# Optimization experiments

Hardware: AMD Instinct MI355X
Metric: run time of the kernel (lower is better)

Reference implementation:

```python
import jax, jax.numpy as jnp
import numpy as np

P, B, FEAT, HID, ATTN, NHEAD = 4096, 32, 512, 512, 512, 8
HD = ATTN // NHEAD  # 64


def setup_inputs() -> dict:
    key = jax.random.key(0)
    ks = jax.random.split(key, 12)
    s = lambda n: 1.0 / np.sqrt(n)
    return {
        "last_hidden": jax.random.normal(ks[0], (1, B, HID), jnp.float32),
        "encoder_outputs": jax.random.normal(ks[1], (P, B, FEAT), jnp.float32),
        # outer projections (stored [in, out]; torch Linear is x @ W.T + b)
        "Wa_w": jax.random.uniform(ks[2], (FEAT, ATTN), jnp.float32, -s(FEAT), s(FEAT)),
        "Wa_b": jax.random.uniform(ks[3], (ATTN,), jnp.float32, -s(FEAT), s(FEAT)),
        "Ua_w": jax.random.uniform(ks[4], (HID, ATTN), jnp.float32, -s(HID), s(HID)),
        "Ua_b": jax.random.uniform(ks[5], (ATTN,), jnp.float32, -s(HID), s(HID)),
        # inner Attention(head_attn_size, head_attn_size, head_attn_size)
        "Wa2_w": jax.random.uniform(ks[6], (HD, HD), jnp.float32, -s(HD), s(HD)),
        "Wa2_b": jax.random.uniform(ks[7], (HD,), jnp.float32, -s(HD), s(HD)),
        "Ua2_w": jax.random.uniform(ks[8], (HD, HD), jnp.float32, -s(HD), s(HD)),
        "Ua2_b": jax.random.uniform(ks[9], (HD,), jnp.float32, -s(HD), s(HD)),
        "va_w": jax.random.uniform(ks[10], (HD, 1), jnp.float32, -s(HD), s(HD)),
        "va_b": jax.random.uniform(ks[11], (1,), jnp.float32, -s(HD), s(HD)),
        "nhead": NHEAD,
    }


def reference(last_hidden, encoder_outputs, Wa_w, Wa_b, Ua_w, Ua_b,
              Wa2_w, Wa2_b, Ua2_w, Ua2_b, va_w, va_b, nhead):
    p, b = encoder_outputs.shape[:2]
    enc = encoder_outputs @ Wa_w + Wa_b            # [P,B,A]
    hid = last_hidden @ Ua_w + Ua_b                # [1,B,A]
    hd = enc.shape[-1] // nhead
    enc = enc.reshape(p, b, nhead, hd)             # [P,B,nh,hd]
    hid = hid.reshape(1, b, nhead, hd)             # [1,B,nh,hd]
    # inner Bahdanau attention
    a = jnp.tanh((enc @ Wa2_w + Wa2_b) + (hid @ Ua2_w + Ua2_b))
    scores = a @ va_w + va_b                       # [P,B,nh,1]
    weights = jax.nn.softmax(scores, axis=0)       # softmax over pixels
    context = jnp.sum(weights * enc, axis=0, keepdims=True)  # [1,B,nh,hd]
    weight = jnp.mean(weights, axis=-2)            # mean over heads -> [P,B,1]
    context = context.reshape(1, b, nhead * hd)    # [1,B,A]
    return context, weight
```

## Files before the change

### kernel.cpp

```cpp
#include <hip/hip_runtime.h>
#include <hip/hip_bf16.h>

#define PDIM 4096
#define BDIM 32
#define MDIM (PDIM*BDIM)
#define KDIM 512
#define NDIM 512
#define NH   8
#define HD   64

typedef __attribute__((ext_vector_type(4))) float f32x4;
typedef __attribute__((ext_vector_type(8))) short bf16x8;

__device__ __forceinline__ unsigned short f2bf(float f) {
  unsigned u = __float_as_uint(f);
  u += 0x7fffu + ((u >> 16) & 1u);
  return (unsigned short)(u >> 16);
}
__device__ __forceinline__ float bf2f(unsigned short u) {
  return __uint_as_float(((unsigned)u) << 16);
}

__device__ __forceinline__ float fast_tanh(float x) {
  x = fminf(fmaxf(x, -15.f), 15.f);
  float e = __expf(2.f * x);
  return __fdividef(e - 1.f, e + 1.f);
}

#define GLOAD_LDS16(g, l) __builtin_amdgcn_global_load_lds( \
    (const __attribute__((address_space(1))) void*)(g),     \
    (__attribute__((address_space(3))) void*)(l), 16, 0, 0)

__global__ __launch_bounds__(256) void cvt_k(
    const float* __restrict__ x, unsigned short* __restrict__ xbf) {
  size_t i = ((size_t)blockIdx.x * 256 + threadIdx.x) * 8;
  float4 a = *(const float4*)(x + i);
  float4 b = *(const float4*)(x + i + 4);
  ushort4 o0; o0.x = f2bf(a.x); o0.y = f2bf(a.y); o0.z = f2bf(a.z); o0.w = f2bf(a.w);
  ushort4 o1; o1.x = f2bf(b.x); o1.y = f2bf(b.y); o1.z = f2bf(b.z); o1.w = f2bf(b.w);
  *(ushort4*)(xbf + i) = o0;
  *(ushort4*)(xbf + i + 4) = o1;
}

__global__ __launch_bounds__(512) void hub_k(
    const float* __restrict__ lh, const float* __restrict__ Ua,
    const float* __restrict__ Ua_b, const float* __restrict__ Ua2,
    const float* __restrict__ Ua2_b, const float* __restrict__ Wa_b,
    const float* __restrict__ Wa2, const float* __restrict__ Wa2_b,
    float* __restrict__ ubf) {
  int b = blockIdx.x, tid = threadIdx.x;
  __shared__ float ls[512];
  __shared__ float hs[512];
  ls[tid] = lh[b*512 + tid];
  __syncthreads();
  float s = Ua_b[tid];
  #pragma unroll 8
  for (int k = 0; k < 512; ++k)
    s += ls[k] * Ua[(size_t)k*512 + tid];
  hs[tid] = s;
  __syncthreads();
  int h = tid >> 6, j = tid & 63;
  float u = Ua2_b[j] + Wa2_b[j];
  #pragma unroll 4
  for (int k = 0; k < 64; ++k) {
    u += hs[h*64 + k] * Ua2[k*64 + j];
    u += Wa_b[h*64 + k] * Wa2[k*64 + j];
  }
  ubf[b*512 + tid] = u;
}

__global__ __launch_bounds__(256) void wft_k(
    const float* __restrict__ Wa, const float* __restrict__ Wa2,
    unsigned short* __restrict__ WfT) {
  int n = blockIdx.x, tid = threadIdx.x;
  int h = n >> 6, j = n & 63;
  __shared__ float w2[64];
  if (tid < 64) w2[tid] = Wa2[tid*64 + j];
  __syncthreads();
  for (int k = tid; k < 512; k += 256) {
    float s = 0.f;
    #pragma unroll 8
    for (int kk = 0; kk < 64; ++kk)
      s += Wa[(size_t)k*512 + h*64 + kk] * w2[kk];
    WfT[(size_t)n*512 + k] = f2bf(s);
  }
}

__global__ __launch_bounds__(256, 4) void gemm_score_k(
    const unsigned short* __restrict__ xbf, const unsigned short* __restrict__ WfT,
    const float* __restrict__ ubf, const float* __restrict__ va_w,
    const float* __restrict__ va_b, float* __restrict__ scores) {
  __shared__ __align__(16) unsigned short sm[16384];
  unsigned short* As = sm;
  unsigned short* Bs = sm + 8192;
  int tid = threadIdx.x;
  int orig = blockIdx.x;
  int wg = (orig & 7) * 512 + (orig >> 3);
  int bn = wg & 3, bm = wg >> 2;
  int m0 = bm*128, n0 = bn*128;
  int lane = tid & 63, w = tid >> 6;
  int quad = lane >> 4, l16 = lane & 15;
  int wr = w >> 1, wc = w & 1;
  int xr = (l16 & 7) << 4;
  f32x4 acc[4][4] = {};

  for (int k0 = 0; k0 < KDIM; k0 += 64) {
    __syncthreads();
    #pragma unroll
    for (int i = 0; i < 4; ++i) {
      int c = i*256 + tid;
      int r = c >> 3, kc = (c & 7) ^ (r & 7);
      GLOAD_LDS16(xbf + (size_t)(m0 + r)*512 + k0 + kc*8, As + (size_t)c*8);
    }
    #pragma unroll
    for (int i = 0; i < 4; ++i) {
      int c = i*256 + tid;
      int r = c >> 3, kc = (c & 7) ^ (r & 7);
      GLOAD_LDS16(WfT + (size_t)(n0 + r)*512 + k0 + kc*8, Bs + (size_t)c*8);
    }
    __syncthreads();
    #pragma unroll
    for (int kk = 0; kk < 64; kk += 32) {
      int kc = (kk >> 3) + quad;
      bf16x8 af[4], bfr[4];
      #pragma unroll
      for (int ti = 0; ti < 4; ++ti) {
        int row = 64*wr + 16*ti + l16;
        af[ti] = *(const bf16x8*)((const char*)As + ((row*128 + kc*16) ^ xr));
      }
      #pragma unroll
      for (int tj = 0; tj < 4; ++tj) {
        int row = 64*wc + 16*tj + l16;
        bfr[tj] = *(const bf16x8*)((const char*)Bs + ((row*128 + kc*16) ^ xr));
      }
      #pragma unroll
      for (int ti = 0; ti < 4; ++ti)
        #pragma unroll
        for (int tj = 0; tj < 4; ++tj)
          acc[ti][tj] = __builtin_amdgcn_mfma_f32_16x16x32_bf16(
              af[ti], bfr[tj], acc[ti][tj], 0, 0, 0);
    }
  }

  __syncthreads();
  float* ubf_s = (float*)sm;
  #pragma unroll
  for (int t = 0; t < 16; ++t) {
    int idx = t*256 + tid;
    int b = idx >> 7, c = idx & 127;
    ubf_s[b*129 + c] = ubf[b*512 + n0 + c];
  }
  __syncthreads();

  int head = bn*2 + wc;
  float va_r[4];
  #pragma unroll
  for (int tj = 0; tj < 4; ++tj) va_r[tj] = va_w[16*tj + l16];
  float vb = va_b[0];
  #pragma unroll
  for (int ti = 0; ti < 4; ++ti) {
    #pragma unroll
    for (int r = 0; r < 4; ++r) {
      int row_loc = 64*wr + 16*ti + 4*quad + r;
      int b31 = row_loc & 31;
      float s = 0.f;
      #pragma unroll
      for (int tj = 0; tj < 4; ++tj) {
        float xa = acc[ti][tj][r] + ubf_s[b31*129 + 64*wc + 16*tj + l16];
        s += fast_tanh(xa) * va_r[tj];
      }
      s += __shfl_xor(s, 1); s += __shfl_xor(s, 2);
      s += __shfl_xor(s, 4); s += __shfl_xor(s, 8);
      if (l16 == 0) {
        int m = m0 + row_loc;
        scores[((size_t)head*32 + (m & 31))*4096 + (m >> 5)] = s + vb;
      }
    }
  }
}

__global__ __launch_bounds__(256) void softmax_k(
    const float* __restrict__ sc, float* __restrict__ w) {
  int bh = blockIdx.x;
  int tid = threadIdx.x;
  const float* row = sc + (size_t)bh*4096;
  float4 v[4];
  float mx = -1e30f;
  #pragma unroll
  for (int i = 0; i < 4; ++i) {
    v[i] = *(const float4*)(row + (size_t)(i*256 + tid)*4);
    mx = fmaxf(mx, fmaxf(fmaxf(v[i].x, v[i].y), fmaxf(v[i].z, v[i].w)));
  }
  #pragma unroll
  for (int m = 1; m < 64; m <<= 1) mx = fmaxf(mx, __shfl_xor(mx, m));
  __shared__ float redm[4], reds[4];
  int wid = tid >> 6, lane = tid & 63;
  if (lane == 0) redm[wid] = mx;
  __syncthreads();
  mx = fmaxf(fmaxf(redm[0], redm[1]), fmaxf(redm[2], redm[3]));
  float sum = 0.f;
  #pragma unroll
  for (int i = 0; i < 4; ++i) {
    v[i].x = __expf(v[i].x - mx); v[i].y = __expf(v[i].y - mx);
    v[i].z = __expf(v[i].z - mx); v[i].w = __expf(v[i].w - mx);
    sum += v[i].x + v[i].y + v[i].z + v[i].w;
  }
  #pragma unroll
  for (int m = 1; m < 64; m <<= 1) sum += __shfl_xor(sum, m);
  if (lane == 0) reds[wid] = sum;
  __syncthreads();
  sum = reds[0] + reds[1] + reds[2] + reds[3];
  float inv = 1.f / sum;
  float* dst = w + (size_t)bh*4096;
  #pragma unroll
  for (int i = 0; i < 4; ++i) {
    float4 o; o.x = v[i].x*inv; o.y = v[i].y*inv; o.z = v[i].z*inv; o.w = v[i].w*inv;
    *(float4*)(dst + (size_t)(i*256 + tid)*4) = o;
  }
}

__global__ __launch_bounds__(256) void mean_k(
    const float* __restrict__ w, float* __restrict__ out) {
  int p0 = blockIdx.x * 256;
  int tid = threadIdx.x;
  float s[32];
  #pragma unroll
  for (int b = 0; b < 32; ++b) s[b] = 0.f;
  for (int h = 0; h < 8; ++h) {
    #pragma unroll
    for (int b = 0; b < 32; ++b)
      s[b] += w[((size_t)h*32 + b)*4096 + p0 + tid];
  }
  float4* dst = (float4*)(out + BDIM*NDIM + (size_t)(p0 + tid)*32);
  #pragma unroll
  for (int j = 0; j < 8; ++j) {
    float4 o;
    o.x = s[4*j]*0.125f; o.y = s[4*j+1]*0.125f;
    o.z = s[4*j+2]*0.125f; o.w = s[4*j+3]*0.125f;
    dst[j] = o;
  }
}

__global__ __launch_bounds__(256) void ctx_partial_k(
    const unsigned short* __restrict__ xbf, const float* __restrict__ w,
    float* __restrict__ part) {
  int pc = blockIdx.x;
  int b  = blockIdx.y;
  int tid = threadIdx.x;
  __shared__ float wl[8*256];
  __shared__ float red[4][512];
  #pragma unroll
  for (int h = 0; h < 8; ++h)
    wl[h*256 + tid] = w[((size_t)h*32 + b)*4096 + pc*256 + tid];
  __syncthreads();
  int lane = tid & 63, wv = tid >> 6;
  float acc[8][8];
  #pragma unroll
  for (int h = 0; h < 8; ++h)
    #pragma unroll
    for (int j = 0; j < 8; ++j) acc[h][j] = 0.f;
  for (int i = 0; i < 64; ++i) {
    int pl = wv*64 + i;
    bf16x8 xv = *(const bf16x8*)(xbf + ((size_t)((pc*256 + pl)*32 + b))*512 + lane*8);
    float xf[8];
    #pragma unroll
    for (int j = 0; j < 8; ++j) xf[j] = bf2f((unsigned short)xv[j]);
    #pragma unroll
    for (int h = 0; h < 8; ++h) {
      float ww = wl[h*256 + pl];
      #pragma unroll
      for (int j = 0; j < 8; ++j) acc[h][j] += ww * xf[j];
    }
  }
  for (int h = 0; h < 8; ++h) {
    #pragma unroll
    for (int j = 0; j < 8; j += 4)
      *(float4*)(&red[wv][lane*8 + j]) = *(float4*)(&acc[h][j]);
    __syncthreads();
    if (tid < 64) {
      #pragma unroll
      for (int j = 0; j < 8; ++j) {
        int f = tid*8 + j;
        part[((size_t)(b*16 + pc)*NH + h)*512 + f] =
            red[0][f] + red[1][f] + red[2][f] + red[3][f];
      }
    }
    __syncthreads();
  }
}

__global__ __launch_bounds__(256) void ctx_reduce_k(
    const float* __restrict__ part, float* __restrict__ cx) {
  int gid = blockIdx.x*256 + threadIdx.x;
  float s = 0.f;
  int f = gid & 511;
  int bh = gid >> 9;
  int h = bh & 7, b = bh >> 3;
  #pragma unroll
  for (int pc = 0; pc < 16; ++pc)
    s += part[((size_t)(b*16 + pc)*NH + h)*512 + f];
  cx[gid] = s;
}

__global__ __launch_bounds__(256) void ctx_proj_k(
    const float* __restrict__ cx, const float* __restrict__ Wa,
    const float* __restrict__ Wa_b, float* __restrict__ out) {
  int b = blockIdx.x >> 3, h = blockIdx.x & 7;
  int tid = threadIdx.x;
  __shared__ float cs[512];
  cs[tid]       = cx[(size_t)blockIdx.x*512 + tid];
  cs[tid + 256] = cx[(size_t)blockIdx.x*512 + tid + 256];
  __syncthreads();
  int d = tid & 63, g = tid >> 6;
  float s = 0.f;
  #pragma unroll 8
  for (int f = g*128; f < g*128 + 128; ++f)
    s += cs[f] * Wa[(size_t)f*512 + h*64 + d];
  __shared__ float red[256];
  red[tid] = s;
  __syncthreads();
  if (tid < 64) {
    float tot = red[tid] + red[64+tid] + red[128+tid] + red[192+tid] + Wa_b[h*64 + tid];
    out[b*512 + h*64 + tid] = tot;
  }
}

extern "C" void kernel_launch(void* const* d_in, const int* in_sizes, int n_in,
                              void* d_out, int out_size, void* d_ws, size_t ws_size,
                              hipStream_t stream) {
  (void)in_sizes; (void)n_in; (void)out_size; (void)ws_size;
  const float* lh    = (const float*)d_in[0];
  const float* x     = (const float*)d_in[1];
  const float* Wa_w  = (const float*)d_in[2];
  const float* Wa_b  = (const float*)d_in[3];
  const float* Ua_w  = (const float*)d_in[4];
  const float* Ua_b  = (const float*)d_in[5];
  const float* Wa2_w = (const float*)d_in[6];
  const float* Wa2_b = (const float*)d_in[7];
  const float* Ua2_w = (const float*)d_in[8];
  const float* Ua2_b = (const float*)d_in[9];
  const float* va_w  = (const float*)d_in[10];
  const float* va_b  = (const float*)d_in[11];
  float* out = (float*)d_out;
  char* ws = (char*)d_ws;

  unsigned short* xbf = (unsigned short*)(ws);
  unsigned short* WfT = (unsigned short*)(ws + 134217728);
  float* ubf    = (float*)(ws + 134742016);
  float* scores = (float*)(ws + 134807552);
  float* w      = (float*)(ws + 139001856);
  float* part   = (float*)(ws + 143196160);
  float* cx     = (float*)(ws + 151584768);

  hipLaunchKernelGGL(cvt_k, dim3(32768), dim3(256), 0, stream, x, xbf);
  hipLaunchKernelGGL(hub_k, dim3(32), dim3(512), 0, stream,
                     lh, Ua_w, Ua_b, Ua2_w, Ua2_b, Wa_b, Wa2_w, Wa2_b, ubf);
  hipLaunchKernelGGL(wft_k, dim3(512), dim3(256), 0, stream, Wa_w, Wa2_w, WfT);
  hipLaunchKernelGGL(gemm_score_k, dim3(4096), dim3(256), 0, stream,
                     xbf, WfT, ubf, va_w, va_b, scores);
  hipLaunchKernelGGL(softmax_k, dim3(256), dim3(256), 0, stream, scores, w);
  hipLaunchKernelGGL(mean_k, dim3(16), dim3(256), 0, stream, w, out);
  hipLaunchKernelGGL(ctx_partial_k, dim3(16, 32), dim3(256), 0, stream, xbf, w, part);
  hipLaunchKernelGGL(ctx_reduce_k, dim3(512), dim3(256), 0, stream, part, cx);
  hipLaunchKernelGGL(ctx_proj_k, dim3(256), dim3(256), 0, stream, cx, Wa_w, Wa_b, out);
}
```

Measured before the change: 597.0 us.

## Fuse fp32-to-bf16 conversion into GEMM A-load and merge small prep/reduce kernels

```diff
diff --git a/kernel.cpp b/kernel.cpp
--- a/kernel.cpp
+++ b/kernel.cpp
@@ -31,63 +31,52 @@
     (const __attribute__((address_space(1))) void*)(g),     \
     (__attribute__((address_space(3))) void*)(l), 16, 0, 0)
 
-__global__ __launch_bounds__(256) void cvt_k(
-    const float* __restrict__ x, unsigned short* __restrict__ xbf) {
-  size_t i = ((size_t)blockIdx.x * 256 + threadIdx.x) * 8;
-  float4 a = *(const float4*)(x + i);
-  float4 b = *(const float4*)(x + i + 4);
-  ushort4 o0; o0.x = f2bf(a.x); o0.y = f2bf(a.y); o0.z = f2bf(a.z); o0.w = f2bf(a.w);
-  ushort4 o1; o1.x = f2bf(b.x); o1.y = f2bf(b.y); o1.z = f2bf(b.z); o1.w = f2bf(b.w);
-  *(ushort4*)(xbf + i) = o0;
-  *(ushort4*)(xbf + i + 4) = o1;
-}
-
-__global__ __launch_bounds__(512) void hub_k(
+__global__ __launch_bounds__(512) void prep_k(
+    const float* __restrict__ Wa, const float* __restrict__ Wa2,
+    unsigned short* __restrict__ WfT,
     const float* __restrict__ lh, const float* __restrict__ Ua,
     const float* __restrict__ Ua_b, const float* __restrict__ Ua2,
     const float* __restrict__ Ua2_b, const float* __restrict__ Wa_b,
-    const float* __restrict__ Wa2, const float* __restrict__ Wa2_b,
-    float* __restrict__ ubf) {
-  int b = blockIdx.x, tid = threadIdx.x;
-  __shared__ float ls[512];
-  __shared__ float hs[512];
-  ls[tid] = lh[b*512 + tid];
-  __syncthreads();
-  float s = Ua_b[tid];
-  #pragma unroll 8
-  for (int k = 0; k < 512; ++k)
-    s += ls[k] * Ua[(size_t)k*512 + tid];
-  hs[tid] = s;
-  __syncthreads();
-  int h = tid >> 6, j = tid & 63;
-  float u = Ua2_b[j] + Wa2_b[j];
-  #pragma unroll 4
-  for (int k = 0; k < 64; ++k) {
-    u += hs[h*64 + k] * Ua2[k*64 + j];
-    u += Wa_b[h*64 + k] * Wa2[k*64 + j];
-  }
-  ubf[b*512 + tid] = u;
-}
-
-__global__ __launch_bounds__(256) void wft_k(
-    const float* __restrict__ Wa, const float* __restrict__ Wa2,
-    unsigned short* __restrict__ WfT) {
-  int n = blockIdx.x, tid = threadIdx.x;
-  int h = n >> 6, j = n & 63;
-  __shared__ float w2[64];
-  if (tid < 64) w2[tid] = Wa2[tid*64 + j];
-  __syncthreads();
-  for (int k = tid; k < 512; k += 256) {
+    const float* __restrict__ Wa2_b, float* __restrict__ ubf) {
+  int tid = threadIdx.x;
+  if (blockIdx.x < 512) {
+    int n = blockIdx.x;
+    int h = n >> 6, j = n & 63;
+    __shared__ float w2[64];
+    if (tid < 64) w2[tid] = Wa2[tid*64 + j];
+    __syncthreads();
+    int k = tid;
     float s = 0.f;
     #pragma unroll 8
     for (int kk = 0; kk < 64; ++kk)
       s += Wa[(size_t)k*512 + h*64 + kk] * w2[kk];
     WfT[(size_t)n*512 + k] = f2bf(s);
+  } else {
+    int b = blockIdx.x - 512;
+    __shared__ float ls[512];
+    __shared__ float hs[512];
+    ls[tid] = lh[b*512 + tid];
+    __syncthreads();
+    float s = Ua_b[tid];
+    #pragma unroll 8
+    for (int k = 0; k < 512; ++k)
+      s += ls[k] * Ua[(size_t)k*512 + tid];
+    hs[tid] = s;
+    __syncthreads();
+    int h = tid >> 6, j = tid & 63;
+    float u = Ua2_b[j] + Wa2_b[j];
+    #pragma unroll 4
+    for (int k = 0; k < 64; ++k) {
+      u += hs[h*64 + k] * Ua2[k*64 + j];
+      u += Wa_b[h*64 + k] * Wa2[k*64 + j];
+    }
+    ubf[b*512 + tid] = u;
   }
 }
 
 __global__ __launch_bounds__(256, 4) void gemm_score_k(
-    const unsigned short* __restrict__ xbf, const unsigned short* __restrict__ WfT,
+    const float* __restrict__ x, unsigned short* __restrict__ xbf,
+    const unsigned short* __restrict__ WfT,
     const float* __restrict__ ubf, const float* __restrict__ va_w,
     const float* __restrict__ va_b, float* __restrict__ scores) {
   __shared__ __align__(16) unsigned short sm[16384];
@@ -110,13 +99,32 @@
     for (int i = 0; i < 4; ++i) {
       int c = i*256 + tid;
       int r = c >> 3, kc = (c & 7) ^ (r & 7);
-      GLOAD_LDS16(xbf + (size_t)(m0 + r)*512 + k0 + kc*8, As + (size_t)c*8);
-    }
-    #pragma unroll
-    for (int i = 0; i < 4; ++i) {
-      int c = i*256 + tid;
-      int r = c >> 3, kc = (c & 7) ^ (r & 7);
       GLOAD_LDS16(WfT + (size_t)(n0 + r)*512 + k0 + kc*8, Bs + (size_t)c*8);
+    }
+    #pragma unroll
+    for (int half = 0; half < 2; ++half) {
+      float4 av[2][2];
+      #pragma unroll
+      for (int i = 0; i < 2; ++i) {
+        int p = (half*2 + i)*256 + tid;
+        int r = p >> 3, c8 = p & 7;
+        const float4* s = (const float4*)(x + (size_t)(m0 + r)*512 + k0 + c8*8);
+        av[i][0] = s[0]; av[i][1] = s[1];
+      }
+      #pragma unroll
+      for (int i = 0; i < 2; ++i) {
+        int p = (half*2 + i)*256 + tid;
+        int r = p >> 3, c8 = p & 7;
+        bf16x8 v;
+        v[0] = (short)f2bf(av[i][0].x); v[1] = (short)f2bf(av[i][0].y);
+        v[2] = (short)f2bf(av[i][0].z); v[3] = (short)f2bf(av[i][0].w);
+        v[4] = (short)f2bf(av[i][1].x); v[5] = (short)f2bf(av[i][1].y);
+        v[6] = (short)f2bf(av[i][1].z); v[7] = (short)f2bf(av[i][1].w);
+        if (bn == 0)
+          *(bf16x8*)(xbf + (size_t)(m0 + r)*512 + k0 + c8*8) = v;
+        int slot = c8 ^ (r & 7);
+        *(bf16x8*)(As + (size_t)(r*8 + slot)*8) = v;
+      }
     }
     __syncthreads();
     #pragma unroll
@@ -289,27 +297,21 @@
   }
 }
 
-__global__ __launch_bounds__(256) void ctx_reduce_k(
-    const float* __restrict__ part, float* __restrict__ cx) {
-  int gid = blockIdx.x*256 + threadIdx.x;
-  float s = 0.f;
-  int f = gid & 511;
-  int bh = gid >> 9;
-  int h = bh & 7, b = bh >> 3;
-  #pragma unroll
-  for (int pc = 0; pc < 16; ++pc)
-    s += part[((size_t)(b*16 + pc)*NH + h)*512 + f];
-  cx[gid] = s;
-}
-
-__global__ __launch_bounds__(256) void ctx_proj_k(
-    const float* __restrict__ cx, const float* __restrict__ Wa,
+__global__ __launch_bounds__(256) void ctx_rp_k(
+    const float* __restrict__ part, const float* __restrict__ Wa,
     const float* __restrict__ Wa_b, float* __restrict__ out) {
-  int b = blockIdx.x >> 3, h = blockIdx.x & 7;
+  int bh = blockIdx.x;
+  int b = bh >> 3, h = bh & 7;
   int tid = threadIdx.x;
   __shared__ float cs[512];
-  cs[tid]       = cx[(size_t)blockIdx.x*512 + tid];
-  cs[tid + 256] = cx[(size_t)blockIdx.x*512 + tid + 256];
+  float s0 = 0.f, s1 = 0.f;
+  #pragma unroll
+  for (int pc = 0; pc < 16; ++pc) {
+    const float* p = part + ((size_t)(b*16 + pc)*NH + h)*512;
+    s0 += p[tid];
+    s1 += p[tid + 256];
+  }
+  cs[tid] = s0; cs[tid + 256] = s1;
   __syncthreads();
   int d = tid & 63, g = tid >> 6;
   float s = 0.f;
@@ -351,16 +353,15 @@
   float* w      = (float*)(ws + 139001856);
   float* part   = (float*)(ws + 143196160);
   float* cx     = (float*)(ws + 151584768);
-
-  hipLaunchKernelGGL(cvt_k, dim3(32768), dim3(256), 0, stream, x, xbf);
-  hipLaunchKernelGGL(hub_k, dim3(32), dim3(512), 0, stream,
-                     lh, Ua_w, Ua_b, Ua2_w, Ua2_b, Wa_b, Wa2_w, Wa2_b, ubf);
-  hipLaunchKernelGGL(wft_k, dim3(512), dim3(256), 0, stream, Wa_w, Wa2_w, WfT);
+  (void)cx;
+
+  hipLaunchKernelGGL(prep_k, dim3(544), dim3(512), 0, stream,
+                     Wa_w, Wa2_w, WfT,
+                     lh, Ua_w, Ua_b, Ua2_w, Ua2_b, Wa_b, Wa2_b, ubf);
   hipLaunchKernelGGL(gemm_score_k, dim3(4096), dim3(256), 0, stream,
-                     xbf, WfT, ubf, va_w, va_b, scores);
+                     x, xbf, WfT, ubf, va_w, va_b, scores);
   hipLaunchKernelGGL(softmax_k, dim3(256), dim3(256), 0, stream, scores, w);
   hipLaunchKernelGGL(mean_k, dim3(16), dim3(256), 0, stream, w, out);
   hipLaunchKernelGGL(ctx_partial_k, dim3(16, 32), dim3(256), 0, stream, xbf, w, part);
-  hipLaunchKernelGGL(ctx_reduce_k, dim3(512), dim3(256), 0, stream, part, cx);
-  hipLaunchKernelGGL(ctx_proj_k, dim3(256), dim3(256), 0, stream, cx, Wa_w, Wa_b, out);
-}
+  hipLaunchKernelGGL(ctx_rp_k, dim3(256), dim3(256), 0, stream, part, Wa_w, Wa_b, out);
+}
```

Result: no change. 597.7 us (+0.1%).
